# Optimization experiments

Hardware: AMD Instinct MI355X
Metric: run time of the kernel (lower is better)

The kernel has to match this reference:

```python
import jax, jax.numpy as jnp
import numpy as np
from jax import lax


def _zc_rmsnorm(x, w, eps=1e-6):
    # ZeroCentredRMSNorm: scale is (1 + weight), weight init zeros
    v = jnp.mean(jnp.square(x), -1, keepdims=True)
    return x * lax.rsqrt(v + eps) * (1.0 + w)


def _short_conv(x, w, seg_id):
    # Depthwise causal conv (kernel=4, torch Conv1d tap layout) + silu,
    # respecting packed-segment boundaries (contributions from other
    # segments are masked out, matching varlen causal_conv1d).
    T = x.shape[0]
    out = x * w[:, 3]
    for s in range(1, 4):
        shifted = jnp.pad(x, ((s, 0), (0, 0)))[:T]
        same = jnp.pad(seg_id, (s, 0), constant_values=-1)[:T] == seg_id
        out = out + jnp.where(same[:, None], shifted, 0.0) * w[:, 3 - s]
    return jax.nn.silu(out)


def _l2norm(x, eps=1e-6):
    return x * lax.rsqrt(jnp.sum(jnp.square(x), -1, keepdims=True) + eps)


def _forward(x, ac_table, W_in, b_in, norm_w, Wq, Wk, Wv, conv_qw, conv_kw,
             conv_vw, Wb, Wa, A_log, dt_bias, Wg, o_norm_w, Wo, W_head, b_head,
             cu_seqlens, aircraft_type_idx):
    T = x.shape[0]
    NH = A_log.shape[0]
    # segment id per packed token
    seg_id = jnp.searchsorted(cu_seqlens, jnp.arange(T), side='right') - 1
    ac = ac_table[aircraft_type_idx]                    # [S, AC_D]
    h = jnp.concatenate([x, ac[seg_id]], axis=1) @ W_in + b_in  # [T, H]
    residual = h
    hn = _zc_rmsnorm(h, norm_w)
    # GatedDeltaNet projections + short conv + silu
    q = _short_conv(hn @ Wq, conv_qw, seg_id)           # [T, KD]
    k = _short_conv(hn @ Wk, conv_kw, seg_id)           # [T, KD]
    v = _short_conv(hn @ Wv, conv_vw, seg_id)           # [T, VD]
    HK = q.shape[1] // NH
    HV = v.shape[1] // NH
    q = _l2norm(q.reshape(T, NH, HK))
    k = _l2norm(k.reshape(T, NH, HK))
    v = v.reshape(T, NH, HV)
    beta = jax.nn.sigmoid(hn @ Wb)                      # [T, NH]
    g = -jnp.exp(A_log) * jax.nn.softplus(hn @ Wa + dt_bias)  # [T, NH] log-decay
    scale = HK ** -0.5
    # reset flag: 1.0 at the first token of each segment
    starts = jnp.zeros((T,), jnp.float32).at[cu_seqlens[:-1]].set(1.0)

    def step(S, inp):
        qt, kt, vt, gt, bt, rt = inp
        S = S * (1.0 - rt) * jnp.exp(gt)[:, None, None]       # decay (+ reset)
        kv = jnp.einsum('hk,hkv->hv', kt, S)                   # S^T k
        S = S + kt[:, :, None] * (bt[:, None] * (vt - kv))[:, None, :]
        return S, jnp.einsum('hk,hkv->hv', qt, S)

    S0 = jnp.zeros((NH, HK, HV), jnp.float32)
    _, o = lax.scan(step, S0, (q * scale, k, v, g, beta, starts))  # o: [T,NH,HV]
    # swish-gated RMSNorm on output heads
    gate = (hn @ Wg).reshape(T, NH, HV)
    o = o * lax.rsqrt(jnp.mean(jnp.square(o), -1, keepdims=True) + 1e-5) * o_norm_w
    o = o * gate * jax.nn.sigmoid(gate)
    h = o.reshape(T, NH * HV) @ Wo + residual
    pooled = h[cu_seqlens[1:] - 1]                      # 'last' pooling
    return pooled @ W_head + b_head                     # [S, 1]


def setup_inputs() -> dict:
    T, D_IN, H, NH, AC_N, AC_D, S = 32768, 16, 1024, 12, 64, 32, 16
    KD = int(H * 0.75)          # 768
    VD = KD * 2                 # 1536 (expand_v = 2)
    HK, HV = KD // NH, VD // NH # 64, 128
    rng = np.random.default_rng(0)
    interior = np.sort(rng.choice(np.arange(1, T), S - 1, replace=False))
    cu = jnp.asarray(np.concatenate([[0], interior, [T]]).astype(np.int32))
    ks = jax.random.split(jax.random.key(0), 24)

    def n(i, shape, s=0.02):
        return jax.random.normal(ks[i], shape, jnp.float32) * s

    return dict(
        x=jax.random.normal(ks[0], (T, D_IN), jnp.float32),
        cu_seqlens=cu,
        aircraft_type_idx=jax.random.randint(ks[1], (S,), 0, AC_N),
        ac_table=n(2, (AC_N, AC_D), 1.0),
        W_in=n(3, (D_IN + AC_D, H)), b_in=jnp.zeros((H,), jnp.float32),
        norm_w=jnp.zeros((H,), jnp.float32),
        Wq=n(4, (H, KD)), Wk=n(5, (H, KD)), Wv=n(6, (H, VD)),
        conv_qw=n(7, (KD, 4), 0.2), conv_kw=n(8, (KD, 4), 0.2),
        conv_vw=n(9, (VD, 4), 0.2),
        Wb=n(10, (H, NH)), Wa=n(11, (H, NH)),
        A_log=jnp.log(jax.random.uniform(ks[12], (NH,), jnp.float32, 1.0, 16.0)),
        dt_bias=n(13, (NH,), 0.1),
        Wg=n(14, (H, VD)), o_norm_w=jnp.ones((HV,), jnp.float32),
        Wo=n(15, (VD, H)),
        W_head=n(16, (H, 1)), b_head=jnp.zeros((1,), jnp.float32),
    )


def reference(x, cu_seqlens, aircraft_type_idx, ac_table, W_in, b_in, norm_w,
              Wq, Wk, Wv, conv_qw, conv_kw, conv_vw, Wb, Wa, A_log, dt_bias,
              Wg, o_norm_w, Wo, W_head, b_head):
    return _forward(x, ac_table, W_in, b_in, norm_w, Wq, Wk, Wv, conv_qw,
                    conv_kw, conv_vw, Wb, Wa, A_log, dt_bias, Wg, o_norm_w,
                    Wo, W_head, b_head, cu_seqlens, aircraft_type_idx)
```

## Files before the change

kernel.cpp:

```cpp
#include <hip/hip_runtime.h>
#include <stdint.h>

#define T_TOK 32768
#define H_DIM 1024
#define NH    12
#define HK    64
#define HV    128
#define KD    768
#define VD    1536
#define NSEG  16
#define NCOL  2432
#define FEAT  48
#define CHUNK_M 4096
#define NSLOT (T_TOK/8 + 32)
#define MAXSB 96
#define OCH   8

typedef unsigned int uint;
typedef unsigned short ushort;

typedef short bf16x8_t __attribute__((ext_vector_type(8)));
typedef float f32x4_t  __attribute__((ext_vector_type(4)));

__device__ __forceinline__ ushort f2b(float f){
  uint u = __float_as_uint(f);
  u += 0x7fffu + ((u>>16)&1u);
  return (ushort)(u>>16);
}
__device__ __forceinline__ float b2f(ushort u){ return __uint_as_float(((uint)u)<<16); }
__device__ __forceinline__ void unpack2(uint u, float&a, float&b){
  a = __uint_as_float(u<<16); b = __uint_as_float(u & 0xffff0000u);
}
__device__ __forceinline__ float sigm(float x){ return 1.f/(1.f + __expf(-x)); }
__device__ __forceinline__ float silu(float x){ return x * sigm(x); }

__global__ void segk(const int* __restrict__ cu, int* __restrict__ seg){
  int t = blockIdx.x*256 + threadIdx.x;
  if (t >= T_TOK) return;
  int s = 0;
  #pragma unroll
  for (int i=1;i<=NSEG;i++) s += (cu[i] <= t) ? 1 : 0;
  seg[t] = s;
}

__global__ __launch_bounds__(256,1) void stage_a(const float* __restrict__ x,
   const int* __restrict__ atype, const float* __restrict__ ac_table,
   const float* __restrict__ W_in, const float* __restrict__ b_in,
   const float* __restrict__ norm_w, const int* __restrict__ seg, int row_base,
   ushort* __restrict__ hn, float* __restrict__ h_end, float* __restrict__ hn_ends)
{
  __shared__ float feat[8][FEAT];
  __shared__ float hbuf[8][H_DIM];
  __shared__ float red[8];
  int tid = threadIdx.x;
  int base = row_base + blockIdx.x*8;
  int lbase = blockIdx.x*8;
  if (tid < 8) red[tid] = 0.f;
  for (int idx=tid; idx<8*FEAT; idx+=256){
    int rr = idx / FEAT, i = idx % FEAT;
    int t = base + rr;
    float v;
    if (i < 16) v = x[t*16 + i];
    else { int s = seg[t]; int a = atype[s]; v = ac_table[a*32 + (i-16)]; }
    feat[rr][i] = v;
  }
  __syncthreads();
  int c0 = tid*4;
  int lane = tid & 63;
  float4 bi = *(const float4*)&b_in[c0];
  for (int rc=0; rc<2; rc++){
    float acc[4][4];
    #pragma unroll
    for (int r4=0;r4<4;r4++){ acc[r4][0]=bi.x; acc[r4][1]=bi.y; acc[r4][2]=bi.z; acc[r4][3]=bi.w; }
    for (int i=0;i<FEAT;i++){
      float4 wu = *(const float4*)&W_in[i*H_DIM + c0];
      #pragma unroll
      for (int r4=0;r4<4;r4++){
        float f = feat[rc*4+r4][i];
        acc[r4][0] = fmaf(f,wu.x,acc[r4][0]);
        acc[r4][1] = fmaf(f,wu.y,acc[r4][1]);
        acc[r4][2] = fmaf(f,wu.z,acc[r4][2]);
        acc[r4][3] = fmaf(f,wu.w,acc[r4][3]);
      }
    }
    #pragma unroll
    for (int r4=0;r4<4;r4++){
      int rr = rc*4+r4;
      float sq = acc[r4][0]*acc[r4][0] + acc[r4][1]*acc[r4][1]
               + acc[r4][2]*acc[r4][2] + acc[r4][3]*acc[r4][3];
      #pragma unroll
      for (int off=1; off<64; off<<=1) sq += __shfl_xor(sq, off);
      if (lane==0) atomicAdd(&red[rr], sq);
      hbuf[rr][c0]=acc[r4][0]; hbuf[rr][c0+1]=acc[r4][1];
      hbuf[rr][c0+2]=acc[r4][2]; hbuf[rr][c0+3]=acc[r4][3];
    }
  }
  __syncthreads();
  float4 nw = *(const float4*)&norm_w[c0];
  for (int rr=0; rr<8; rr++){
    int t = base + rr;
    float sc = rsqrtf(red[rr]*(1.f/1024.f) + 1e-6f);
    float h0=hbuf[rr][c0], h1=hbuf[rr][c0+1], h2=hbuf[rr][c0+2], h3=hbuf[rr][c0+3];
    float n0=h0*sc*(1.f+nw.x), n1=h1*sc*(1.f+nw.y);
    float n2=h2*sc*(1.f+nw.z), n3=h3*sc*(1.f+nw.w);
    uint2 ov; ov.x = (uint)f2b(n0) | ((uint)f2b(n1)<<16);
    ov.y = (uint)f2b(n2) | ((uint)f2b(n3)<<16);
    *(uint2*)&hn[(size_t)(lbase+rr)*H_DIM + c0] = ov;
    int sgt = seg[t];
    bool isend = (t == T_TOK-1) || (seg[t+1] != sgt);
    if (isend){
      float* he = h_end + (size_t)sgt*H_DIM + c0;
      he[0]=h0; he[1]=h1; he[2]=h2; he[3]=h3;
    }
    #pragma unroll
    for (int d=0; d<4; d++){
      int td = t + d;
      if (td < T_TOK && seg[td] == sgt){
        bool end2 = (td == T_TOK-1) || (seg[td+1] != sgt);
        if (end2){
          float* hd = hn_ends + ((size_t)sgt*4 + (3-d))*H_DIM + c0;
          hd[0]=n0; hd[1]=n1; hd[2]=n2; hd[3]=n3;
        }
      }
    }
  }
}

__global__ void build_wt(const float* __restrict__ Wk, const float* __restrict__ Wv,
                         const float* __restrict__ Wb, const float* __restrict__ Wa,
                         ushort* __restrict__ wt)
{
  int idx = blockIdx.x*256 + threadIdx.x;
  int n = idx >> 10, k = idx & 1023;
  float v;
  if      (n < 768)  v = Wk[k*768 + n];
  else if (n < 2304) v = Wv[k*1536 + (n-768)];
  else if (n < 2316) v = Wb[k*12 + (n-2304)];
  else if (n < 2328) v = Wa[k*12 + (n-2316)];
  else               v = 0.f;
  wt[idx] = f2b(v);
}

__global__ __launch_bounds__(256,1) void gemm_bf16(const ushort* __restrict__ A,
    const ushort* __restrict__ Bt, int row_base,
    ushort* __restrict__ kpre, ushort* __restrict__ vpre, float* __restrict__ ba)
{
  const int K = H_DIM;
  __shared__ ushort As[128*40];
  __shared__ ushort Bs[128*40];
  int tid = threadIdx.x;
  const int ntile = NCOL >> 7;
  int mt = blockIdx.x / ntile, nt = blockIdx.x % ntile;
  int m0 = mt<<7, n0 = nt<<7;
  int r = tid>>2, c8 = (tid&3)<<3;
  const ushort* pa0 = A  + (size_t)(m0 + r)*K + c8;
  const ushort* pa1 = A  + (size_t)(m0 + r + 64)*K + c8;
  const ushort* pb0 = Bt + (size_t)(n0 + r)*K + c8;
  const ushort* pb1 = Bt + (size_t)(n0 + r + 64)*K + c8;
  int lane = tid & 63;
  int wv = tid >> 6; int wm = (wv>>1)<<6, wn = (wv&1)<<6;
  int mloc = lane & 15, q8 = (lane>>4)<<3;
  f32x4_t acc[4][4];
  f32x4_t zero = {0.f,0.f,0.f,0.f};
  #pragma unroll
  for (int i=0;i<4;i++)
    #pragma unroll
    for (int j=0;j<4;j++) acc[i][j] = zero;
  for (int kk=0; kk<K; kk+=32){
    uint4 a0 = *(const uint4*)(pa0 + kk);
    uint4 a1 = *(const uint4*)(pa1 + kk);
    uint4 b0 = *(const uint4*)(pb0 + kk);
    uint4 b1 = *(const uint4*)(pb1 + kk);
    __syncthreads();
    *(uint4*)&As[r*40 + c8] = a0;
    *(uint4*)&As[(r+64)*40 + c8] = a1;
    *(uint4*)&Bs[r*40 + c8] = b0;
    *(uint4*)&Bs[(r+64)*40 + c8] = b1;
    __syncthreads();
    bf16x8_t af[4], bfr[4];
    #pragma unroll
    for (int i=0;i<4;i++){
      af[i]  = *(const bf16x8_t*)&As[(wm + i*16 + mloc)*40 + q8];
      bfr[i] = *(const bf16x8_t*)&Bs[(wn + i*16 + mloc)*40 + q8];
    }
    #pragma unroll
    for (int i=0;i<4;i++)
      #pragma unroll
      for (int j=0;j<4;j++)
        acc[i][j] = __builtin_amdgcn_mfma_f32_16x16x32_bf16(af[i], bfr[j], acc[i][j], 0,0,0);
  }
  int rq = (lane>>4)<<2;
  if (nt < 18){
    ushort* dst; int nstr, cbase;
    if (nt < 6) { dst = kpre; nstr = KD; cbase = n0; }
    else        { dst = vpre; nstr = VD; cbase = n0 - KD; }
    #pragma unroll
    for (int i=0;i<4;i++){
      #pragma unroll
      for (int j=0;j<4;j++){
        int colg = cbase + wn + j*16 + mloc;
        #pragma unroll
        for (int rg=0; rg<4; rg++){
          int rowg = row_base + m0 + wm + i*16 + rq + rg;
          dst[(size_t)rowg*nstr + colg] = f2b(acc[i][j][rg]);
        }
      }
    }
  } else {
    #pragma unroll
    for (int i=0;i<4;i++){
      #pragma unroll
      for (int j=0;j<4;j++){
        int cl = wn + j*16 + mloc;
        if (cl >= 24) continue;
        #pragma unroll
        for (int rg=0; rg<4; rg++){
          int rowg = row_base + m0 + wm + i*16 + rq + rg;
          ba[(size_t)rowg*32 + cl] = acc[i][j][rg];
        }
      }
    }
  }
}

__global__ void dbk(const float* __restrict__ ba, const float* __restrict__ A_log,
                    const float* __restrict__ dt_bias, float2* __restrict__ db)
{
  int idx = blockIdx.x*256 + threadIdx.x;
  if (idx >= T_TOK*NH) return;
  int t = idx / NH, hh = idx % NH;
  float bp = ba[(size_t)t*32 + hh];
  float ap = ba[(size_t)t*32 + 12 + hh] + dt_bias[hh];
  float beta = sigm(bp);
  float sp = (ap > 20.f) ? ap : log1pf(__expf(ap));
  float dec = __expf(-__expf(A_log[hh]) * sp);
  float2 o; o.x = dec; o.y = beta;
  db[idx] = o;
}

__global__ void side_k(const ushort* __restrict__ kpre, const ushort* __restrict__ vpre,
                       ushort* __restrict__ side)
{
  int b = blockIdx.x;
  int base = b*64;
  for (int idx=threadIdx.x; idx<3*2304; idx+=256){
    int jrow = idx / 2304, c = idx % 2304;
    int t0 = base - 3 + jrow;
    ushort v = 0;
    if (t0 >= 0)
      v = (c < KD) ? kpre[(size_t)t0*KD + c] : vpre[(size_t)t0*VD + (c-KD)];
    side[(size_t)(b*3 + jrow)*2304 + c] = v;
  }
}

__global__ __launch_bounds__(256,1) void conv_ip(ushort* __restrict__ kpre,
   ushort* __restrict__ vpre, const ushort* __restrict__ side,
   const int* __restrict__ seg, const float* __restrict__ ckw, const float* __restrict__ cvw)
{
  int tid = threadIdx.x;
  int b = blockIdx.x;
  int base = b * 64;
  float w[9][4];
  int cj[9];
  #pragma unroll
  for (int j=0;j<9;j++){
    int c = tid + 256*j;
    cj[j] = c;
    float4 wu = (c < KD) ? *(const float4*)&ckw[c*4] : *(const float4*)&cvw[(c-KD)*4];
    w[j][0]=wu.x; w[j][1]=wu.y; w[j][2]=wu.z; w[j][3]=wu.w;
  }
  float p[9][4];
  #pragma unroll
  for (int j=0;j<9;j++){
    p[j][1] = b2f(side[(size_t)(b*3+0)*2304 + cj[j]]);
    p[j][2] = b2f(side[(size_t)(b*3+1)*2304 + cj[j]]);
    p[j][3] = b2f(side[(size_t)(b*3+2)*2304 + cj[j]]);
  }
  int s1 = (base-3>=0) ? seg[base-3] : -1;
  int s2 = (base-2>=0) ? seg[base-2] : -1;
  int s3 = (base-1>=0) ? seg[base-1] : -1;
  int s0;
  for (int rr=0; rr<64; rr++){
    int t = base + rr;
    s0 = s1; s1 = s2; s2 = s3; s3 = seg[t];
    #pragma unroll
    for (int j=0;j<9;j++){
      p[j][0]=p[j][1]; p[j][1]=p[j][2]; p[j][2]=p[j][3];
      int c = cj[j];
      p[j][3] = (c < KD) ? b2f(kpre[(size_t)t*KD + c]) : b2f(vpre[(size_t)t*VD + (c-KD)]);
    }
    bool m0 = (s0==s3), m1 = (s1==s3), m2 = (s2==s3);
    #pragma unroll
    for (int j=0;j<9;j++){
      float val = p[j][3]*w[j][3];
      val += m2 ? p[j][2]*w[j][2] : 0.f;
      val += m1 ? p[j][1]*w[j][1] : 0.f;
      val += m0 ? p[j][0]*w[j][0] : 0.f;
      val = silu(val);
      int c = cj[j];
      if (j < 3){
        float sq = val*val;
        #pragma unroll
        for (int off=1; off<64; off<<=1) sq += __shfl_xor(sq, off);
        float kn = val * rsqrtf(sq + 1e-6f);
        kpre[(size_t)t*KD + c] = f2b(kn);
      } else {
        vpre[(size_t)t*VD + (c-KD)] = f2b(val);
      }
    }
  }
}

__global__ __launch_bounds__(256,1) void qpre_k(const float* __restrict__ hn_ends,
   const float* __restrict__ Wq, const int* __restrict__ cu, float* __restrict__ qpre)
{
  __shared__ float hrow[H_DIM];
  int tid = threadIdx.x;
  int s = blockIdx.x >> 2, rr = blockIdx.x & 3;
  int t = cu[s+1] - 4 + rr;
  if (t >= 0)
    *(float4*)&hrow[tid*4] = *(const float4*)&hn_ends[(size_t)(s*4+rr)*H_DIM + tid*4];
  __syncthreads();
  for (int j=0;j<3;j++){
    int c = tid + 256*j;
    float acc = 0.f;
    if (t >= 0){
      for (int i0=0; i0<H_DIM; i0++)
        acc = fmaf(hrow[i0], Wq[(size_t)i0*KD + c], acc);
    }
    qpre[(size_t)(s*4+rr)*KD + c] = acc;
  }
}

__global__ __launch_bounds__(256,1) void qfin_k(const float* __restrict__ qpre,
   const float* __restrict__ cqw, const int* __restrict__ cu, const int* __restrict__ seg,
   float* __restrict__ qf)
{
  int tid = threadIdx.x;
  int s = blockIdx.x;
  int te = cu[s+1]-1;
  for (int j=0;j<3;j++){
    int c = tid + 256*j;
    float4 wu = *(const float4*)&cqw[c*4];
    float wv_[4] = {wu.x, wu.y, wu.z, wu.w};
    float val = 0.f;
    #pragma unroll
    for (int rr=0; rr<4; rr++){
      int t = te - 3 + rr;
      bool ok = (t >= 0) && (seg[t] == s);
      float pv = qpre[(size_t)(s*4+rr)*KD + c];
      val += ok ? pv * wv_[rr] : 0.f;
    }
    val = silu(val);
    float sq = val*val;
    #pragma unroll
    for (int off=1; off<64; off<<=1) sq += __shfl_xor(sq, off);
    qf[(size_t)s*KD + c] = val * rsqrtf(sq + 1e-6f) * 0.125f;
  }
}

__global__ __launch_bounds__(64,1) void gq_k(const ushort* __restrict__ kpost,
   const float2* __restrict__ db, const int* __restrict__ cu, float* __restrict__ gbuf)
{
  __shared__ float kls[8][64];
  __shared__ float dls[8];
  __shared__ float bls[8];
  int slot = blockIdx.x, h = blockIdx.y;
  int s=-1, n=0, te=0, L=0, st0=0;
  for (int ss=0; ss<NSEG; ss++){
    int st = cu[ss], en = cu[ss+1];
    int base = (st>>3) + ss;
    int nb = (en - st + 7) >> 3;
    if (slot >= base && slot < base + nb){ s=ss; n=slot-base; te=en-1; L=en-st; st0=st; }
  }
  if (s < 0) return;
  int lane = threadIdx.x;
  int vl = lane>>3, kq = lane&7;
  int j = 8*n + vl;
  bool ok = j < L;
  int t = ok ? (te - j) : st0;
  uint4 kv = *(const uint4*)(kpost + (size_t)t*KD + h*HK + kq*8);
  float f0,f1,f2,f3,f4,f5,f6,f7;
  unpack2(kv.x,f0,f1); unpack2(kv.y,f2,f3); unpack2(kv.z,f4,f5); unpack2(kv.w,f6,f7);
  if (!ok){ f0=0;f1=0;f2=0;f3=0;f4=0;f5=0;f6=0;f7=0; }
  float4 w0; w0.x=f0; w0.y=f1; w0.z=f2; w0.w=f3;
  float4 w1; w1.x=f4; w1.y=f5; w1.z=f6; w1.w=f7;
  *(float4*)&kls[vl][kq*8]   = w0;
  *(float4*)&kls[vl][kq*8+4] = w1;
  if (kq==0){
    float dd = 1.f, bb = 0.f;
    if (ok){ float2 g = db[(size_t)t*NH + h]; dd = g.x; bb = g.y; }
    dls[vl] = dd; bls[vl] = bb;
  }
  __syncthreads();
  float out = 0.f;
  if (lane < 28){
    int i = 1, base = 0;
    while (lane >= base + i){ base += i; i++; }
    int m = lane - base;
    const float4* pm = (const float4*)kls[m];
    const float4* pi = (const float4*)kls[i];
    float g = 0.f;
    #pragma unroll
    for (int d=0; d<16; d++){
      float4 xa = pm[d], xb = pi[d];
      g += xa.x*xb.x + xa.y*xb.y + xa.z*xb.z + xa.w*xb.w;
    }
    float W = 1.f;
    for (int l=m; l<i; l++) W *= dls[l];
    out = W * bls[m] * g;
  } else if (lane < 36){
    int i0 = lane - 28;
    float P = 1.f;
    for (int l=0; l<=i0; l++) P *= dls[l];
    out = P;
  } else if (lane < 44){
    int m = lane - 36;
    float W = 1.f;
    for (int l=m; l<8; l++) W *= dls[l];
    out = W * bls[m];
  } else if (lane < 52){
    out = bls[lane-44];
  }
  if (lane < 52) gbuf[((size_t)slot*NH + h)*52 + lane] = out;
}

__device__ __forceinline__ int sb_locate(const int* cu, int slot,
   int& m, int& start, int& te, int& L, int& gb)
{
  int acc = 0;
  int sfound = -1;
  for (int ss=0; ss<NSEG; ss++){
    int st = cu[ss], en = cu[ss+1];
    int Ls = en - st, nb8 = (Ls+7)>>3, nsb = (nb8+63)>>6;
    if (slot >= acc && slot < acc + nsb){
      sfound = ss; m = slot - acc; start = st; te = en-1; L = Ls; gb = (st>>3)+ss;
    }
    acc += nsb;
  }
  return sfound;
}

__global__ __launch_bounds__(512,1) void msb_k(const ushort* __restrict__ kpost,
   const float* __restrict__ gbuf, const int* __restrict__ cu, float* __restrict__ mbuf)
{
  __shared__ float kls[2][8][64];
  int slot = blockIdx.x, h = blockIdx.y;
  int m, start, te, L, gb;
  int s = sb_locate(cu, slot, m, start, te, L, gb);
  if (s < 0) return;
  int nb8 = (L+7)>>3;
  int n0 = m*64, n1 = min(nb8, n0+64);
  int tid = threadIdx.x;
  int lane = tid & 63;
  int wv = tid >> 6;
  int cl = lane >> 3, kq = lane & 7;
  int col = wv*8 + cl;
  int d0 = kq*8;
  const ushort* kbase = kpost + h*HK;
  float r0 = (d0+0==col)?1.f:0.f, r1 = (d0+1==col)?1.f:0.f;
  float r2 = (d0+2==col)?1.f:0.f, r3 = (d0+3==col)?1.f:0.f;
  float r4 = (d0+4==col)?1.f:0.f, r5 = (d0+5==col)?1.f:0.f;
  float r6 = (d0+6==col)?1.f:0.f, r7 = (d0+7==col)?1.f:0.f;
  {
    int jj = 8*n0 + wv; int td = (jj<L) ? (te-jj) : start;
    kls[0][wv][lane] = b2f(kbase[(size_t)td*KD + lane]);
  }
  __syncthreads();
  int buf = 0;
  for (int n=n0; n<n1; n++){
    {
      int nn = (n+1<n1) ? n+1 : n;
      int jj = 8*nn + wv; int td = (jj<L) ? (te-jj) : start;
      kls[buf^1][wv][lane] = b2f(kbase[(size_t)td*KD + lane]);
    }
    const float4* g4 = (const float4*)(gbuf + ((size_t)(gb+n)*NH + h)*52);
    float4 q0=g4[0], q1=g4[1], q2=g4[2], q3=g4[3], q4=g4[4], q5=g4[5], q6=g4[6],
           q7=g4[7], q8=g4[8], q9=g4[9], q10=g4[10];
    float a0,a1,a2,a3,a4,a5,a6,a7;
#define DOTJ(J, A) { \
    float4 ka = *(const float4*)&kls[buf][J][d0]; \
    float4 kbv = *(const float4*)&kls[buf][J][d0+4]; \
    float xx = ka.x*r0 + ka.y*r1; \
    xx = fmaf(ka.z, r2, xx); xx = fmaf(ka.w, r3, xx); \
    xx = fmaf(kbv.x, r4, xx); xx = fmaf(kbv.y, r5, xx); \
    xx = fmaf(kbv.z, r6, xx); xx = fmaf(kbv.w, r7, xx); \
    A = xx; }
    DOTJ(0,a0) DOTJ(1,a1) DOTJ(2,a2) DOTJ(3,a3)
    DOTJ(4,a4) DOTJ(5,a5) DOTJ(6,a6) DOTJ(7,a7)
#undef DOTJ
    a0 += __shfl_xor(a0,1); a1 += __shfl_xor(a1,1); a2 += __shfl_xor(a2,1); a3 += __shfl_xor(a3,1);
    a4 += __shfl_xor(a4,1); a5 += __shfl_xor(a5,1); a6 += __shfl_xor(a6,1); a7 += __shfl_xor(a7,1);
    a0 += __shfl_xor(a0,2); a1 += __shfl_xor(a1,2); a2 += __shfl_xor(a2,2); a3 += __shfl_xor(a3,2);
    a4 += __shfl_xor(a4,2); a5 += __shfl_xor(a5,2); a6 += __shfl_xor(a6,2); a7 += __shfl_xor(a7,2);
    a0 += __shfl_xor(a0,4); a1 += __shfl_xor(a1,4); a2 += __shfl_xor(a2,4); a3 += __shfl_xor(a3,4);
    a4 += __shfl_xor(a4,4); a5 += __shfl_xor(a5,4); a6 += __shfl_xor(a6,4); a7 += __shfl_xor(a7,4);
    float c0 = a0;
    float c1 = q7.x*a1 - q0.x*c0;
    float c2 = q7.y*a2 - q0.y*c0 - q0.z*c1;
    float c3 = q7.z*a3 - q0.w*c0 - q1.x*c1 - q1.y*c2;
    float c4 = q7.w*a4 - q1.z*c0 - q1.w*c1 - q2.x*c2 - q2.y*c3;
    float c5 = q8.x*a5 - q2.z*c0 - q2.w*c1 - q3.x*c2 - q3.y*c3 - q3.z*c4;
    float c6 = q8.y*a6 - q3.w*c0 - q4.x*c1 - q4.y*c2 - q4.z*c3 - q4.w*c4 - q5.x*c5;
    float c7 = q8.z*a7 - q5.y*c0 - q5.z*c1 - q5.w*c2 - q6.x*c3 - q6.y*c4 - q6.z*c5 - q6.w*c6;
    float g0 = q9.x*c0, g1 = q9.y*c1, g2 = q9.z*c2, g3 = q9.w*c3;
    float g4_= q10.x*c4, g5 = q10.y*c5, g6 = q10.z*c6, g7 = q10.w*c7;
    float P8 = q8.w;
    r0*=P8; r1*=P8; r2*=P8; r3*=P8; r4*=P8; r5*=P8; r6*=P8; r7*=P8;
#define UPDJ(J, G) { \
    float4 ka = *(const float4*)&kls[buf][J][d0]; \
    float4 kbv = *(const float4*)&kls[buf][J][d0+4]; \
    r0 = fmaf(-(G), ka.x, r0); r1 = fmaf(-(G), ka.y, r1); \
    r2 = fmaf(-(G), ka.z, r2); r3 = fmaf(-(G), ka.w, r3); \
    r4 = fmaf(-(G), kbv.x, r4); r5 = fmaf(-(G), kbv.y, r5); \
    r6 = fmaf(-(G), kbv.z, r6); r7 = fmaf(-(G), kbv.w, r7); }
    UPDJ(0,g0) UPDJ(1,g1) UPDJ(2,g2) UPDJ(3,g3)
    UPDJ(4,g4_) UPDJ(5,g5) UPDJ(6,g6) UPDJ(7,g7)
#undef UPDJ
    __syncthreads();
    buf ^= 1;
  }
  float* mp = mbuf + ((size_t)slot*NH + h)*4096 + (size_t)col*64 + d0;
  float4 oA; oA.x=r0; oA.y=r1; oA.z=r2; oA.w=r3;
  float4 oB; oB.x=r4; oB.y=r5; oB.z=r6; oB.w=r7;
  *(float4*)&mp[0] = oA;
  *(float4*)&mp[4] = oB;
}

__global__ __launch_bounds__(64,1) void chain_k(const float* __restrict__ mbuf,
   const float* __restrict__ qf, const int* __restrict__ cu, float* __restrict__ rbuf)
{
  __shared__ float lsr[64];
  int bid = blockIdx.x;
  int s = bid / NH, h = bid % NH;
  int start = cu[s], end = cu[s+1];
  int L = end - start, nb8 = (L+7)>>3, nsb = (nb8+63)>>6;
  int sbase = 0;
  for (int ss=0; ss<s; ss++){
    int Ls = cu[ss+1]-cu[ss];
    sbase += ((((Ls+7)>>3)+63)>>6);
  }
  int lane = threadIdx.x;
  lsr[lane] = qf[(size_t)s*KD + h*HK + lane];
  __syncthreads();
  float r[64];
  #pragma unroll
  for (int i=0;i<64;i++) r[i] = lsr[i];
  for (int mm=0; mm<nsb; mm++){
    int slot = sbase + mm;
    rbuf[((size_t)slot*NH + h)*64 + lane] = lsr[lane];
    if (mm+1 >= nsb) break;
    const float* mb = mbuf + ((size_t)slot*NH + h)*4096 + lane;
    float y = 0.f;
    #pragma unroll
    for (int col=0; col<64; col++)
      y = fmaf(mb[(size_t)col*64], r[col], y);
    __syncthreads();
    lsr[lane] = y;
    __syncthreads();
    #pragma unroll
    for (int i=0;i<64;i++) r[i] = lsr[i];
  }
}

__global__ __launch_bounds__(64,1) void scan3_k(const ushort* __restrict__ kpost,
   const float* __restrict__ gbuf, const float* __restrict__ rbuf,
   const int* __restrict__ cu, float* __restrict__ cbuf)
{
  int slot = blockIdx.x, h = blockIdx.y;
  int m, start, te, L, gb;
  int s = sb_locate(cu, slot, m, start, te, L, gb);
  if (s < 0) return;
  int nb8 = (L+7)>>3;
  int n0 = m*64, n1 = min(nb8, n0+64);
  int lane = threadIdx.x;
  int vl = lane>>3, kq = lane&7;
  const float* rp = rbuf + ((size_t)slot*NH + h)*64 + kq*8;
  float4 rA = *(const float4*)rp;
  float4 rB = *(const float4*)(rp+4);
  float r0=rA.x, r1=rA.y, r2=rA.z, r3=rA.w, r4=rB.x, r5=rB.y, r6=rB.z, r7=rB.w;
  const ushort* kb = kpost + h*HK + kq*8;
  for (int n=n0; n<n1; n++){
    const float4* g4 = (const float4*)(gbuf + ((size_t)(gb+n)*NH + h)*52);
    float4 q0=g4[0], q1=g4[1], q2=g4[2], q3=g4[3], q4=g4[4], q5=g4[5], q6=g4[6],
           q7=g4[7], q8=g4[8], q9=g4[9], q10=g4[10], q11=g4[11], q12=g4[12];
    int jj = 8*n + vl;
    bool ok = jj < L;
    int td = ok ? (te - jj) : start;
    uint4 kd = *(const uint4*)(kb + (size_t)td*KD);
    if (!ok){ kd.x=0; kd.y=0; kd.z=0; kd.w=0; }
    int tb = te - 8*n;
    int t0c = max(tb-0, start), t1c = max(tb-1, start), t2c = max(tb-2, start), t3c = max(tb-3, start);
    int t4c = max(tb-4, start), t5c = max(tb-5, start), t6c = max(tb-6, start), t7c = max(tb-7, start);
    uint4 km0 = *(const uint4*)(kb + (size_t)t0c*KD);
    uint4 km1 = *(const uint4*)(kb + (size_t)t1c*KD);
    uint4 km2 = *(const uint4*)(kb + (size_t)t2c*KD);
    uint4 km3 = *(const uint4*)(kb + (size_t)t3c*KD);
    uint4 km4 = *(const uint4*)(kb + (size_t)t4c*KD);
    uint4 km5 = *(const uint4*)(kb + (size_t)t5c*KD);
    uint4 km6 = *(const uint4*)(kb + (size_t)t6c*KD);
    uint4 km7 = *(const uint4*)(kb + (size_t)t7c*KD);
    float kk0,kk1,kk2,kk3,kk4,kk5,kk6,kk7;
    unpack2(kd.x, kk0, kk1); unpack2(kd.y, kk2, kk3);
    unpack2(kd.z, kk4, kk5); unpack2(kd.w, kk6, kk7);
    float pa = r0*kk0, pb = r1*kk1;
    pa = fmaf(r2, kk2, pa); pb = fmaf(r3, kk3, pb);
    pa = fmaf(r4, kk4, pa); pb = fmaf(r5, kk5, pb);
    pa = fmaf(r6, kk6, pa); pb = fmaf(r7, kk7, pb);
    float part = pa + pb;
    part += __shfl_xor(part, 1); part += __shfl_xor(part, 2); part += __shfl_xor(part, 4);
    float a0 = __shfl(part, 0*8+kq), a1 = __shfl(part, 1*8+kq);
    float a2 = __shfl(part, 2*8+kq), a3 = __shfl(part, 3*8+kq);
    float a4 = __shfl(part, 4*8+kq), a5 = __shfl(part, 5*8+kq);
    float a6 = __shfl(part, 6*8+kq), a7 = __shfl(part, 7*8+kq);
    float c0 = a0;
    float c1 = q7.x*a1 - q0.x*c0;
    float c2 = q7.y*a2 - q0.y*c0 - q0.z*c1;
    float c3 = q7.z*a3 - q0.w*c0 - q1.x*c1 - q1.y*c2;
    float c4 = q7.w*a4 - q1.z*c0 - q1.w*c1 - q2.x*c2 - q2.y*c3;
    float c5 = q8.x*a5 - q2.z*c0 - q2.w*c1 - q3.x*c2 - q3.y*c3 - q3.z*c4;
    float c6 = q8.y*a6 - q3.w*c0 - q4.x*c1 - q4.y*c2 - q4.z*c3 - q4.w*c4 - q5.x*c5;
    float c7 = q8.z*a7 - q5.y*c0 - q5.z*c1 - q5.w*c2 - q6.x*c3 - q6.y*c4 - q6.z*c5 - q6.w*c6;
    {
      float cw = vl==0?c0: vl==1?c1: vl==2?c2: vl==3?c3: vl==4?c4: vl==5?c5: vl==6?c6: c7;
      float bw = vl==0?q11.x: vl==1?q11.y: vl==2?q11.z: vl==3?q11.w:
                 vl==4?q12.x: vl==5?q12.y: vl==6?q12.z: q12.w;
      if (kq == 0 && jj < L) cbuf[(size_t)(te-jj)*NH + h] = bw*cw;
    }
    float g0 = q9.x*c0, g1 = q9.y*c1, g2 = q9.z*c2, g3 = q9.w*c3;
    float g4_= q10.x*c4, g5 = q10.y*c5, g6 = q10.z*c6, g7 = q10.w*c7;
    float P8 = q8.w;
    r0*=P8; r1*=P8; r2*=P8; r3*=P8; r4*=P8; r5*=P8; r6*=P8; r7*=P8;
    float e0,e1,e2,e3,e4,e5,e6,e7;
#define UPD(KM,GM) \
    unpack2(KM.x,e0,e1); unpack2(KM.y,e2,e3); unpack2(KM.z,e4,e5); unpack2(KM.w,e6,e7); \
    r0 = fmaf(-GM, e0, r0); r1 = fmaf(-GM, e1, r1); r2 = fmaf(-GM, e2, r2); r3 = fmaf(-GM, e3, r3); \
    r4 = fmaf(-GM, e4, r4); r5 = fmaf(-GM, e5, r5); r6 = fmaf(-GM, e6, r6); r7 = fmaf(-GM, e7, r7);
    UPD(km0,g0) UPD(km1,g1) UPD(km2,g2) UPD(km3,g3)
    UPD(km4,g4_) UPD(km5,g5) UPD(km6,g6) UPD(km7,g7)
#undef UPD
  }
}

__global__ void zerok(float* __restrict__ p, int n){
  int i = blockIdx.x*256 + threadIdx.x;
  if (i < n) p[i] = 0.f;
}

__global__ __launch_bounds__(128,1) void ogemv2_k(const ushort* __restrict__ vpost,
   const float* __restrict__ cbuf, const int* __restrict__ cu, float* __restrict__ obuf)
{
  int bid = blockIdx.x;
  int ch = bid % OCH;
  int sh = bid / OCH;
  int s = sh / NH, h = sh % NH;
  int start = cu[s], end = cu[s+1];
  int L = end - start;
  int clen = (L + OCH - 1) / OCH;
  int t0 = start + ch*clen;
  int t1 = min(end, t0 + clen);
  if (t0 >= t1) return;
  int v = threadIdx.x;
  const ushort* vp = vpost + h*HV + v;
  const float* cp = cbuf + h;
  float o0=0,o1=0,o2=0,o3=0,o4=0,o5=0,o6=0,o7=0;
  int t = t0;
  for (; t+8 <= t1; t+=8){
    o0 = fmaf(cp[(size_t)(t+0)*NH], b2f(vp[(size_t)(t+0)*VD]), o0);
    o1 = fmaf(cp[(size_t)(t+1)*NH], b2f(vp[(size_t)(t+1)*VD]), o1);
    o2 = fmaf(cp[(size_t)(t+2)*NH], b2f(vp[(size_t)(t+2)*VD]), o2);
    o3 = fmaf(cp[(size_t)(t+3)*NH], b2f(vp[(size_t)(t+3)*VD]), o3);
    o4 = fmaf(cp[(size_t)(t+4)*NH], b2f(vp[(size_t)(t+4)*VD]), o4);
    o5 = fmaf(cp[(size_t)(t+5)*NH], b2f(vp[(size_t)(t+5)*VD]), o5);
    o6 = fmaf(cp[(size_t)(t+6)*NH], b2f(vp[(size_t)(t+6)*VD]), o6);
    o7 = fmaf(cp[(size_t)(t+7)*NH], b2f(vp[(size_t)(t+7)*VD]), o7);
  }
  for (; t<t1; t++) o0 = fmaf(cp[(size_t)t*NH], b2f(vp[(size_t)t*VD]), o0);
  float o = ((o0+o1)+(o2+o3)) + ((o4+o5)+(o6+o7));
  atomicAdd(&obuf[(size_t)s*VD + h*HV + v], o);
}

__global__ __launch_bounds__(256,1) void gate_k(const float* __restrict__ obuf,
   const float* __restrict__ hn_ends, const float* __restrict__ Wg,
   const float* __restrict__ onw, const int* __restrict__ cu, float* __restrict__ og)
{
  __shared__ float red[4];
  __shared__ float hrow[H_DIM];
  int tid = threadIdx.x;
  int s = blockIdx.x / 6, ch = blockIdx.x % 6;
  int cc = ch*256 + tid;
  *(float4*)&hrow[tid*4] = *(const float4*)&hn_ends[(size_t)(s*4+3)*H_DIM + tid*4];
  float o = obuf[(size_t)s*VD + cc];
  float sq = o*o;
  #pragma unroll
  for (int off=1; off<64; off<<=1) sq += __shfl_xor(sq, off);
  int wv = tid>>6, lane = tid&63;
  if (lane==0) red[wv] = sq;
  __syncthreads();
  float ssum = (tid<128) ? (red[0]+red[1]) : (red[2]+red[3]);
  float onr = o * rsqrtf(ssum*(1.f/128.f) + 1e-5f) * onw[cc & 127];
  float acc = 0.f;
  for (int i0=0;i0<H_DIM;i0++)
    acc = fmaf(hrow[i0], Wg[(size_t)i0*VD + cc], acc);
  og[(size_t)s*VD + cc] = onr * acc * sigm(acc);
}

__global__ __launch_bounds__(256,1) void final_k(const float* __restrict__ og,
   const float* __restrict__ Wo, const float* __restrict__ h_end,
   const float* __restrict__ W_head, const float* __restrict__ b_head,
   float* __restrict__ out)
{
  __shared__ float ogs[VD];
  __shared__ float redp[4];
  int tid = threadIdx.x;
  int s = blockIdx.x;
  for (int j=tid; j<VD; j+=256) ogs[j] = og[(size_t)s*VD + j];
  __syncthreads();
  int c0 = tid*4;
  float4 hh4 = *(const float4*)&h_end[(size_t)s*H_DIM + c0];
  float acc0 = hh4.x, acc1 = hh4.y, acc2 = hh4.z, acc3 = hh4.w;
  for (int j=0;j<VD;j++){
    float ov = ogs[j];
    float4 wo = *(const float4*)&Wo[(size_t)j*H_DIM + c0];
    acc0 = fmaf(ov,wo.x,acc0); acc1 = fmaf(ov,wo.y,acc1);
    acc2 = fmaf(ov,wo.z,acc2); acc3 = fmaf(ov,wo.w,acc3);
  }
  float4 wh = *(const float4*)&W_head[c0];
  float p = acc0*wh.x + acc1*wh.y + acc2*wh.z + acc3*wh.w;
  #pragma unroll
  for (int off=1; off<64; off<<=1) p += __shfl_xor(p, off);
  int wv = tid>>6, lane = tid&63;
  if (lane==0) redp[wv] = p;
  __syncthreads();
  if (tid==0) out[s] = redp[0]+redp[1]+redp[2]+redp[3] + b_head[0];
}

extern "C" void kernel_launch(void* const* d_in, const int* in_sizes, int n_in,
                              void* d_out, int out_size, void* d_ws, size_t ws_size,
                              hipStream_t stream)
{
  const float* x      = (const float*)d_in[0];
  const int*   cu     = (const int*)  d_in[1];
  const int*   atype  = (const int*)  d_in[2];
  const float* ac_tab = (const float*)d_in[3];
  const float* W_in   = (const float*)d_in[4];
  const float* b_in   = (const float*)d_in[5];
  const float* norm_w = (const float*)d_in[6];
  const float* Wq     = (const float*)d_in[7];
  const float* Wk     = (const float*)d_in[8];
  const float* Wv     = (const float*)d_in[9];
  const float* cqw    = (const float*)d_in[10];
  const float* ckw    = (const float*)d_in[11];
  const float* cvw    = (const float*)d_in[12];
  const float* Wb     = (const float*)d_in[13];
  const float* Wa     = (const float*)d_in[14];
  const float* A_log  = (const float*)d_in[15];
  const float* dt_b   = (const float*)d_in[16];
  const float* Wg     = (const float*)d_in[17];
  const float* onw    = (const float*)d_in[18];
  const float* Wo     = (const float*)d_in[19];
  const float* W_head = (const float*)d_in[20];
  const float* b_head = (const float*)d_in[21];
  float* out = (float*)d_out;

  char* w = (char*)d_ws;
  int*    seg     = (int*)w;     w += (size_t)T_TOK*4;
  float*  h_end   = (float*)w;   w += (size_t)NSEG*H_DIM*4;
  float*  hn_ends = (float*)w;   w += (size_t)NSEG*4*H_DIM*4;
  float*  qpre    = (float*)w;   w += (size_t)NSEG*4*KD*4;
  float*  qf      = (float*)w;   w += (size_t)NSEG*KD*4;
  float*  obuf    = (float*)w;   w += (size_t)NSEG*VD*4;
  float*  og      = (float*)w;   w += (size_t)NSEG*VD*4;
  float2* db      = (float2*)w;  w += (size_t)T_TOK*NH*8;
  float*  ba      = (float*)w;   w += (size_t)T_TOK*32*4;
  ushort* wt      = (ushort*)w;  w += (size_t)NCOL*H_DIM*2;
  ushort* side    = (ushort*)w;  w += (size_t)(T_TOK/64)*3*2304*2;
  float*  cbuf    = (float*)w;   w += (size_t)T_TOK*NH*4;
  float*  gbuf    = (float*)w;   w += (size_t)NSLOT*NH*52*4;
  float*  mbuf    = (float*)w;   w += (size_t)MAXSB*NH*4096*4;
  float*  rbuf    = (float*)w;   w += (size_t)MAXSB*NH*64*4;
  ushort* hn_c    = (ushort*)w;  w += (size_t)CHUNK_M*H_DIM*2;
  ushort* kpre    = (ushort*)w;  w += (size_t)T_TOK*KD*2;
  ushort* vpre    = (ushort*)w;  w += (size_t)T_TOK*VD*2;

  hipLaunchKernelGGL(segk,     dim3(T_TOK/256),        dim3(256), 0, stream, cu, seg);
  hipLaunchKernelGGL(build_wt, dim3((NCOL*H_DIM)/256), dim3(256), 0, stream, Wk, Wv, Wb, Wa, wt);
  hipLaunchKernelGGL(zerok,    dim3((NSEG*VD+255)/256),dim3(256), 0, stream, obuf, NSEG*VD);
  for (int c = 0; c < T_TOK/CHUNK_M; c++){
    int row_base = c*CHUNK_M;
    hipLaunchKernelGGL(stage_a,  dim3(CHUNK_M/8), dim3(256), 0, stream,
                       x, atype, ac_tab, W_in, b_in, norm_w, seg, row_base, hn_c, h_end, hn_ends);
    hipLaunchKernelGGL(gemm_bf16, dim3((CHUNK_M/128)*(NCOL/128)), dim3(256), 0, stream,
                       hn_c, wt, row_base, kpre, vpre, ba);
  }
  hipLaunchKernelGGL(dbk,      dim3((T_TOK*NH)/256),   dim3(256), 0, stream, ba, A_log, dt_b, db);
  hipLaunchKernelGGL(side_k,   dim3(T_TOK/64),         dim3(256), 0, stream, kpre, vpre, side);
  hipLaunchKernelGGL(conv_ip,  dim3(T_TOK/64),         dim3(256), 0, stream, kpre, vpre, side, seg, ckw, cvw);
  hipLaunchKernelGGL(qpre_k,   dim3(NSEG*4),           dim3(256), 0, stream, hn_ends, Wq, cu, qpre);
  hipLaunchKernelGGL(qfin_k,   dim3(NSEG),             dim3(256), 0, stream, qpre, cqw, cu, seg, qf);
  hipLaunchKernelGGL(gq_k,     dim3(NSLOT, NH),        dim3(64),  0, stream, kpre, db, cu, gbuf);
  hipLaunchKernelGGL(msb_k,    dim3(MAXSB, NH),        dim3(512), 0, stream, kpre, gbuf, cu, mbuf);
  hipLaunchKernelGGL(chain_k,  dim3(NSEG*NH),          dim3(64),  0, stream, mbuf, qf, cu, rbuf);
  hipLaunchKernelGGL(scan3_k,  dim3(MAXSB, NH),        dim3(64),  0, stream, kpre, gbuf, rbuf, cu, cbuf);
  hipLaunchKernelGGL(ogemv2_k, dim3(NSEG*NH*OCH),      dim3(128), 0, stream, vpre, cbuf, cu, obuf);
  hipLaunchKernelGGL(gate_k,   dim3(NSEG*6),           dim3(256), 0, stream, obuf, hn_ends, Wg, onw, cu, og);
  hipLaunchKernelGGL(final_k,  dim3(NSEG),             dim3(256), 0, stream, og, Wo, h_end, W_head, b_head, out);
}
```

Baseline: 1.593 ms.

## Use direct global-to-LDS loads in GEMM and prefetch next-iteration gate data

Result: slower. 1.691 ms (+6.2%).

```diff
diff --git a/kernel.cpp b/kernel.cpp
--- a/kernel.cpp
+++ b/kernel.cpp
@@ -33,6 +33,12 @@
 }
 __device__ __forceinline__ float sigm(float x){ return 1.f/(1.f + __expf(-x)); }
 __device__ __forceinline__ float silu(float x){ return x * sigm(x); }
+
+__device__ __forceinline__ void gl16(const ushort* g, ushort* l){
+  __builtin_amdgcn_global_load_lds(
+    (const __attribute__((address_space(1))) uint*)g,
+    (__attribute__((address_space(3))) uint*)l, 16, 0, 0);
+}
 
 __global__ void segk(const int* __restrict__ cu, int* __restrict__ seg){
   int t = blockIdx.x*256 + threadIdx.x;
@@ -146,19 +152,25 @@
     ushort* __restrict__ kpre, ushort* __restrict__ vpre, float* __restrict__ ba)
 {
   const int K = H_DIM;
-  __shared__ ushort As[128*40];
-  __shared__ ushort Bs[128*40];
+  __shared__ ushort As[128*32];
+  __shared__ ushort Bs[128*32];
   int tid = threadIdx.x;
   const int ntile = NCOL >> 7;
   int mt = blockIdx.x / ntile, nt = blockIdx.x % ntile;
   int m0 = mt<<7, n0 = nt<<7;
-  int r = tid>>2, c8 = (tid&3)<<3;
-  const ushort* pa0 = A  + (size_t)(m0 + r)*K + c8;
-  const ushort* pa1 = A  + (size_t)(m0 + r + 64)*K + c8;
-  const ushort* pb0 = Bt + (size_t)(n0 + r)*K + c8;
-  const ushort* pb1 = Bt + (size_t)(n0 + r + 64)*K + c8;
   int lane = tid & 63;
-  int wv = tid >> 6; int wm = (wv>>1)<<6, wn = (wv&1)<<6;
+  int wv = tid >> 6;
+  int rS = wv*16 + (lane>>2);
+  int cS = (lane&3)<<3;
+  const ushort* pa0 = A  + (size_t)(m0 + rS)*K + cS;
+  const ushort* pa1 = A  + (size_t)(m0 + rS + 64)*K + cS;
+  const ushort* pb0 = Bt + (size_t)(n0 + rS)*K + cS;
+  const ushort* pb1 = Bt + (size_t)(n0 + rS + 64)*K + cS;
+  ushort* lA0 = &As[wv*512];
+  ushort* lA1 = &As[2048 + wv*512];
+  ushort* lB0 = &Bs[wv*512];
+  ushort* lB1 = &Bs[2048 + wv*512];
+  int wm = (wv>>1)<<6, wn = (wv&1)<<6;
   int mloc = lane & 15, q8 = (lane>>4)<<3;
   f32x4_t acc[4][4];
   f32x4_t zero = {0.f,0.f,0.f,0.f};
@@ -167,21 +179,17 @@
     #pragma unroll
     for (int j=0;j<4;j++) acc[i][j] = zero;
   for (int kk=0; kk<K; kk+=32){
-    uint4 a0 = *(const uint4*)(pa0 + kk);
-    uint4 a1 = *(const uint4*)(pa1 + kk);
-    uint4 b0 = *(const uint4*)(pb0 + kk);
-    uint4 b1 = *(const uint4*)(pb1 + kk);
     __syncthreads();
-    *(uint4*)&As[r*40 + c8] = a0;
-    *(uint4*)&As[(r+64)*40 + c8] = a1;
-    *(uint4*)&Bs[r*40 + c8] = b0;
-    *(uint4*)&Bs[(r+64)*40 + c8] = b1;
+    gl16(pa0 + kk, lA0);
+    gl16(pa1 + kk, lA1);
+    gl16(pb0 + kk, lB0);
+    gl16(pb1 + kk, lB1);
     __syncthreads();
     bf16x8_t af[4], bfr[4];
     #pragma unroll
     for (int i=0;i<4;i++){
-      af[i]  = *(const bf16x8_t*)&As[(wm + i*16 + mloc)*40 + q8];
-      bfr[i] = *(const bf16x8_t*)&Bs[(wn + i*16 + mloc)*40 + q8];
+      af[i]  = *(const bf16x8_t*)&As[(wm + i*16 + mloc)*32 + q8];
+      bfr[i] = *(const bf16x8_t*)&Bs[(wn + i*16 + mloc)*32 + q8];
     }
     #pragma unroll
     for (int i=0;i<4;i++)
@@ -466,6 +474,9 @@
     int jj = 8*n0 + wv; int td = (jj<L) ? (te-jj) : start;
     kls[0][wv][lane] = b2f(kbase[(size_t)td*KD + lane]);
   }
+  const float4* g4 = (const float4*)(gbuf + ((size_t)(gb+n0)*NH + h)*52);
+  float4 q0=g4[0], q1=g4[1], q2=g4[2], q3=g4[3], q4=g4[4], q5=g4[5], q6=g4[6],
+         q7=g4[7], q8=g4[8], q9=g4[9], q10=g4[10];
   __syncthreads();
   int buf = 0;
   for (int n=n0; n<n1; n++){
@@ -474,9 +485,10 @@
       int jj = 8*nn + wv; int td = (jj<L) ? (te-jj) : start;
       kls[buf^1][wv][lane] = b2f(kbase[(size_t)td*KD + lane]);
     }
-    const float4* g4 = (const float4*)(gbuf + ((size_t)(gb+n)*NH + h)*52);
-    float4 q0=g4[0], q1=g4[1], q2=g4[2], q3=g4[3], q4=g4[4], q5=g4[5], q6=g4[6],
-           q7=g4[7], q8=g4[8], q9=g4[9], q10=g4[10];
+    int np = (n+1<n1) ? n+1 : n;
+    const float4* gn = (const float4*)(gbuf + ((size_t)(gb+np)*NH + h)*52);
+    float4 p0=gn[0], p1=gn[1], p2=gn[2], p3=gn[3], p4=gn[4], p5=gn[5], p6=gn[6],
+           p7=gn[7], p8=gn[8], p9=gn[9], p10=gn[10];
     float a0,a1,a2,a3,a4,a5,a6,a7;
 #define DOTJ(J, A) { \
     float4 ka = *(const float4*)&kls[buf][J][d0]; \
@@ -517,6 +529,7 @@
     UPDJ(0,g0) UPDJ(1,g1) UPDJ(2,g2) UPDJ(3,g3)
     UPDJ(4,g4_) UPDJ(5,g5) UPDJ(6,g6) UPDJ(7,g7)
 #undef UPDJ
+    q0=p0; q1=p1; q2=p2; q3=p3; q4=p4; q5=p5; q6=p6; q7=p7; q8=p8; q9=p9; q10=p10;
     __syncthreads();
     buf ^= 1;
   }
@@ -580,15 +593,26 @@
   float4 rB = *(const float4*)(rp+4);
   float r0=rA.x, r1=rA.y, r2=rA.z, r3=rA.w, r4=rB.x, r5=rB.y, r6=rB.z, r7=rB.w;
   const ushort* kb = kpost + h*HK + kq*8;
+  const float4* g4 = (const float4*)(gbuf + ((size_t)(gb+n0)*NH + h)*52);
+  float4 q0=g4[0], q1=g4[1], q2=g4[2], q3=g4[3], q4=g4[4], q5=g4[5], q6=g4[6],
+         q7=g4[7], q8=g4[8], q9=g4[9], q10=g4[10], q11=g4[11], q12=g4[12];
+  uint4 kd;
+  {
+    int jj = 8*n0 + vl; bool ok = jj < L; int td = ok ? te - jj : start;
+    kd = *(const uint4*)(kb + (size_t)td*KD);
+    if (!ok){ kd.x=0; kd.y=0; kd.z=0; kd.w=0; }
+  }
   for (int n=n0; n<n1; n++){
-    const float4* g4 = (const float4*)(gbuf + ((size_t)(gb+n)*NH + h)*52);
-    float4 q0=g4[0], q1=g4[1], q2=g4[2], q3=g4[3], q4=g4[4], q5=g4[5], q6=g4[6],
-           q7=g4[7], q8=g4[8], q9=g4[9], q10=g4[10], q11=g4[11], q12=g4[12];
+    int np = (n+1<n1) ? n+1 : n;
+    const float4* gn = (const float4*)(gbuf + ((size_t)(gb+np)*NH + h)*52);
+    float4 p0=gn[0], p1=gn[1], p2=gn[2], p3=gn[3], p4=gn[4], p5=gn[5], p6=gn[6],
+           p7=gn[7], p8=gn[8], p9=gn[9], p10=gn[10], p11=gn[11], p12=gn[12];
+    uint4 kdn; bool okn;
+    {
+      int jj = 8*np + vl; okn = jj < L; int td = okn ? te - jj : start;
+      kdn = *(const uint4*)(kb + (size_t)td*KD);
+    }
     int jj = 8*n + vl;
-    bool ok = jj < L;
-    int td = ok ? (te - jj) : start;
-    uint4 kd = *(const uint4*)(kb + (size_t)td*KD);
-    if (!ok){ kd.x=0; kd.y=0; kd.z=0; kd.w=0; }
     int tb = te - 8*n;
     int t0c = max(tb-0, start), t1c = max(tb-1, start), t2c = max(tb-2, start), t3c = max(tb-3, start);
     int t4c = max(tb-4, start), t5c = max(tb-5, start), t6c = max(tb-6, start), t7c = max(tb-7, start);
@@ -639,6 +663,9 @@
     UPD(km0,g0) UPD(km1,g1) UPD(km2,g2) UPD(km3,g3)
     UPD(km4,g4_) UPD(km5,g5) UPD(km6,g6) UPD(km7,g7)
 #undef UPD
+    q0=p0; q1=p1; q2=p2; q3=p3; q4=p4; q5=p5; q6=p6; q7=p7; q8=p8; q9=p9; q10=p10; q11=p11; q12=p12;
+    if (!okn){ kdn.x=0; kdn.y=0; kdn.z=0; kdn.w=0; }
+    kd = kdn;
   }
 }
 
```
